# Performance work log

Measured on AMD Instinct MI355X. Metric: run time of the kernel, lower is better.

## Reference

```python
import jax, jax.numpy as jnp
import numpy as np

NPOINT = 1024   # number of sampled centers
NSAMPLE = 32    # neighbors per center
BN_EPS = 1e-5


def setup_inputs() -> dict:
    key = jax.random.key(0)
    ks = jax.random.split(key, 6)
    B, N, C = 8, 4096, 6
    inp = {
        "xyz": jax.random.normal(ks[0], (B, N, 3), jnp.float32),
        "points": jax.random.normal(ks[1], (B, N, C), jnp.float32),
        "W0": jax.random.normal(ks[2], (64, 9), jnp.float32) * 0.1,
        "g0": jnp.ones((64,), jnp.float32),
        "b0": jnp.zeros((64,), jnp.float32),
        "W1": jax.random.normal(ks[3], (64, 64), jnp.float32) * 0.1,
        "g1": jnp.ones((64,), jnp.float32),
        "b1": jnp.zeros((64,), jnp.float32),
        "W2": jax.random.normal(ks[4], (128, 64), jnp.float32) * 0.1,
        "g2": jnp.ones((128,), jnp.float32),
        "b2": jnp.zeros((128,), jnp.float32),
    }
    return inp


def sample_and_group(xyz, points):
    # xyz: [B,N,3], points: [B,N,C]
    B, N, _ = xyz.shape
    stride = N // NPOINT
    new_xyz = xyz[:, ::stride]                      # [B,S,3] deterministic subsample (FPS surrogate)
    # squared pairwise distances via ||a||^2 + ||b||^2 - 2 a.b  -> [B,S,N]
    d = (jnp.sum(new_xyz * new_xyz, -1)[:, :, None]
         + jnp.sum(xyz * xyz, -1)[:, None, :]
         - 2.0 * jnp.einsum('bsd,bnd->bsn', new_xyz, xyz))
    _, idx = jax.lax.top_k(-d, NSAMPLE)             # [B,S,K] KNN indices
    gather = jax.vmap(lambda arr, i: arr[i])        # per-batch gather: [N,C],[S,K] -> [S,K,C]
    g_xyz = gather(xyz, idx) - new_xyz[:, :, None, :]   # relative coords [B,S,K,3]
    g_pts = gather(points, idx)                     # [B,S,K,C]
    new_points = jnp.concatenate([g_xyz, g_pts], -1)    # [B,S,K,3+C]
    return new_xyz, new_points


def mlp_layer(x, W, g, b):
    # Conv2d(1x1, bias=False) == channel contraction; BN2d with batch stats; ReLU
    x = jnp.einsum('bskc,oc->bsko', x, W)
    m = jnp.mean(x, axis=(0, 1, 2))
    v = jnp.var(x, axis=(0, 1, 2))
    x = (x - m) * jax.lax.rsqrt(v + BN_EPS) * g + b
    return jax.nn.relu(x)


def reference(xyz, points, W0, g0, b0, W1, g1, b1, W2, g2, b2):
    new_xyz, x = sample_and_group(xyz, points)      # x: [B,S,K,9]
    x = mlp_layer(x, W0, g0, b0)
    x = mlp_layer(x, W1, g1, b1)
    x = mlp_layer(x, W2, g2, b2)
    new_points = jnp.max(x, axis=2)                 # max-pool over neighbor dim K -> [B,S,128]
    return new_xyz, new_points
```

## Files before the change

### kernel.cpp

```cpp
#include <hip/hip_runtime.h>
#include <float.h>
#include <stdint.h>

#define TOT   262144
#define NPTS  4096
#define KNN   32
#define BN_EPS 1e-5f
#define CAPV  64

typedef _Float16 f16;
typedef _Float16 f16x2 __attribute__((ext_vector_type(2)));
typedef _Float16 f16x4 __attribute__((ext_vector_type(4)));
typedef _Float16 f16x8 __attribute__((ext_vector_type(8)));
typedef float    f32x4 __attribute__((ext_vector_type(4)));

__device__ __forceinline__ int mbcnt64(unsigned long long m){
  return __builtin_amdgcn_mbcnt_hi((unsigned)(m>>32),
         __builtin_amdgcn_mbcnt_lo((unsigned)(m & 0xffffffffull), 0));
}
__device__ __forceinline__ unsigned f2ord(float f){
  unsigned u = __float_as_uint(f);
  return u ^ (((unsigned)((int)u >> 31)) | 0x80000000u);
}
__device__ __forceinline__ f16x2 bnrelu2(f16x2 x, f16x2 a, f16x2 c){
  f16x2 r = x*a + c;
  const f16 z = (f16)0.f;
  r[0] = r[0] > z ? r[0] : z;
  r[1] = r[1] > z ? r[1] : z;
  return r;
}

__global__ __launch_bounds__(256) void prep(const float* __restrict__ xyz,
    float4* __restrict__ xyzp){
  int p = blockIdx.x*256 + threadIdx.x;
  float x = xyz[p*3+0], y = xyz[p*3+1], z = xyz[p*3+2];
  xyzp[p] = make_float4(x, y, z, x*x+y*y+z*z);
}

__global__ __launch_bounds__(256) void knn_gather(
    const float4* __restrict__ xyzp, const float* __restrict__ pts,
    float* __restrict__ grouped, float* __restrict__ out_newxyz){
  __shared__ unsigned skey[4*CAPV];
  __shared__ unsigned short sidx[4*CAPV];
  const int lane = threadIdx.x & 63;
  const int wv   = threadIdx.x >> 6;
  const int q = blockIdx.x*4 + wv;
  const int b = q >> 10, s = q & 1023;
  const float4* xb = xyzp + b*NPTS;
  const float4 Q = xb[s*4];
  const float qx=Q.x, qy=Q.y, qz=Q.z, qq=Q.w;
  if (lane==0){ out_newxyz[q*3]=qx; out_newxyz[q*3+1]=qy; out_newxyz[q*3+2]=qz; }

  unsigned m = 0xFFFFFFFFu;
  #pragma unroll 8
  for (int j=0;j<64;j++){
    float4 P = xb[j*64+lane];
    float d = (qq+P.w) - 2.f*(qx*P.x+qy*P.y+qz*P.z);
    unsigned k = f2ord(d);
    m = k<m ? k : m;
  }
  unsigned sm = m;
  #pragma unroll
  for (int k=2;k<=64;k<<=1){
    #pragma unroll
    for (int j=k>>1;j>0;j>>=1){
      unsigned o = __shfl_xor(sm, j, 64);
      bool keepmin = (((lane&k)==0) == ((lane&j)==0));
      sm = keepmin ? (sm<o?sm:o) : (sm>o?sm:o);
    }
  }
  const unsigned U = __shfl(sm, 31, 64);

  unsigned* wk = skey + wv*CAPV;
  unsigned short* wi = sidx + wv*CAPV;
  int cnt = 0;
  #pragma unroll 4
  for (int j=0;j<64;j++){
    float4 P = xb[j*64+lane];
    float d = (qq+P.w) - 2.f*(qx*P.x+qy*P.y+qz*P.z);
    unsigned k = f2ord(d);
    bool sel = (k <= U);
    unsigned long long msk = __ballot(sel);
    int pos = cnt + mbcnt64(msk);
    if (sel && pos < CAPV){ wk[pos]=k; wi[pos]=(unsigned short)(j*64+lane); }
    cnt += __popcll(msk);
  }

  const float* fb = pts + (size_t)b*NPTS*6;
  const int ebase = q*KNN;
  int n = -1;

  if (cnt <= CAPV){
    unsigned myk = (lane<cnt) ? wk[lane] : 0xFFFFFFFFu;
    unsigned myi = (lane<cnt) ? wi[lane] : 0u;
    unsigned long long v = (((unsigned long long)myk)<<16) | myi;
    #pragma unroll
    for (int k=2;k<=64;k<<=1){
      #pragma unroll
      for (int j=k>>1;j>0;j>>=1){
        unsigned long long o = __shfl_xor(v, j, 64);
        bool keepmin = (((lane&k)==0) == ((lane&j)==0));
        v = keepmin ? (v<o?v:o) : (v>o?v:o);
      }
    }
    if (lane < KNN) n = (int)(v & 0xffffull);
  } else {
    unsigned V=0;
    for (int bit=31; bit>=0; --bit){
      unsigned X = V | (1u<<bit);
      int c=0;
      for (int j=0;j<64;j++){
        float4 P = xb[j*64+lane];
        float d = (qq+P.w) - 2.f*(qx*P.x+qy*P.y+qz*P.z);
        c += __popcll(__ballot(f2ord(d) < X));
      }
      if (c < KNN) V = X;
    }
    int cnt2=0;
    for (int pass=0; pass<2; ++pass){
      for (int j=0;j<64;j++){
        float4 P = xb[j*64+lane];
        float d = (qq+P.w) - 2.f*(qx*P.x+qy*P.y+qz*P.z);
        unsigned kk = f2ord(d);
        bool sel = pass ? (kk==V) : (kk<V);
        unsigned long long msk = __ballot(sel);
        int pos = cnt2 + mbcnt64(msk);
        if (sel && pos < KNN){
          int nn = j*64+lane, e = ebase+pos;
          grouped[0*TOT+e]=P.x-qx; grouped[1*TOT+e]=P.y-qy; grouped[2*TOT+e]=P.z-qz;
          for (int c6=0;c6<6;c6++) grouped[(3+c6)*TOT+e]=fb[nn*6+c6];
        }
        cnt2 += __popcll(msk);
      }
    }
  }
  if (n >= 0){
    float4 P = xb[n];
    int e = ebase + lane;
    grouped[0*TOT+e]=P.x-qx; grouped[1*TOT+e]=P.y-qy; grouped[2*TOT+e]=P.z-qz;
    #pragma unroll
    for (int c6=0;c6<6;c6++) grouped[(3+c6)*TOT+e]=fb[n*6+c6];
  }
}

__global__ __launch_bounds__(256) void stats0(
    const float* __restrict__ grouped, float* __restrict__ s0g){
  const int tid = threadIdx.x, lane = tid&63, wv = tid>>6;
  float v[54];
  #pragma unroll
  for (int i=0;i<54;i++) v[i]=0.f;
  #pragma unroll 1
  for (int it=0; it<2; ++it){
    int n = it*(512*256) + blockIdx.x*256 + tid;
    float g[9];
    #pragma unroll
    for (int c=0;c<9;c++) g[c] = grouped[c*TOT+n];
    #pragma unroll
    for (int c=0;c<9;c++) v[c] += g[c];
    int t=9;
    #pragma unroll
    for (int c=0;c<9;c++)
      #pragma unroll
      for (int c2=0;c2<=c;c2++){ v[t] += g[c]*g[c2]; t++; }
  }
  __shared__ float lds[4][54];
  #pragma unroll
  for (int i=0;i<54;i++){
    float r = v[i];
    #pragma unroll
    for (int off=32; off; off>>=1) r += __shfl_xor(r, off, 64);
    if (lane==0) lds[wv][i]=r;
  }
  __syncthreads();
  if (tid < 54) atomicAdd(&s0g[tid], lds[0][tid]+lds[1][tid]+lds[2][tid]+lds[3][tid]);
}

__global__ void finalize0(const float* __restrict__ s0g,
    const float* __restrict__ W0, const float* __restrict__ g0,
    const float* __restrict__ b0, float* __restrict__ ac0,
    const float* __restrict__ W1, const float* __restrict__ W2,
    f16* __restrict__ W0h, f16* __restrict__ W1h, f16* __restrict__ W2h){
  const int tid = threadIdx.x;
  __shared__ float S[54];
  __shared__ float A0s[64];
  if (tid < 54) S[tid] = s0g[tid];
  __syncthreads();
  if (tid < 64){
    float w[9];
    #pragma unroll
    for (int c=0;c<9;c++) w[c]=W0[tid*9+c];
    float m=0.f;
    #pragma unroll
    for (int c=0;c<9;c++) m += w[c]*S[c];
    float e2=0.f; int t=9;
    #pragma unroll
    for (int c=0;c<9;c++)
      #pragma unroll
      for (int c2=0;c2<=c;c2++){
        float x = w[c]*w[c2]*S[t++];
        e2 += (c2==c) ? x : 2.f*x;
      }
    const float inv = 1.f/(float)TOT;
    m *= inv; e2 *= inv;
    float var = e2 - m*m;
    float a = g0[tid]*rsqrtf(var + BN_EPS);
    ac0[tid]    = a;
    ac0[64+tid] = fmaf(-m, a, b0[tid]);
    A0s[tid]    = a;
  }
  __syncthreads();
  for (int i=tid; i<2048; i+=256){
    int o = i>>5, c = i&31;
    W0h[i] = (f16)(c<9 ? A0s[o]*W0[o*9+c] : 0.f);
  }
  for (int i=tid; i<4096; i+=256) W1h[i] = (f16)W1[i];
  for (int i=tid; i<8192; i+=256) W2h[i] = (f16)W2[i];
}

__global__ __launch_bounds__(256) void layer1(
    const float* __restrict__ grouped, const f16* __restrict__ W0h,
    const f16* __restrict__ W1h, const float* __restrict__ ac0,
    f16* __restrict__ x1h){
  __shared__ f16 hb[4][16][80];
  const int lane = threadIdx.x & 63, wv = threadIdx.x >> 6;
  const int e16 = lane & 15, q = lane >> 4;
  const int base = blockIdx.x*256 + wv*64;

  f16x8 A0[4];
  #pragma unroll
  for (int m=0;m<4;m++) A0[m] = *(const f16x8*)(W0h + (m*16+e16)*32 + q*8);
  f16x8 A1[4][2];
  #pragma unroll
  for (int m=0;m<4;m++)
    #pragma unroll
    for (int s=0;s<2;s++) A1[m][s] = *(const f16x8*)(W1h + (m*16+e16)*64 + s*32 + q*8);
  float c0i[4][4];
  #pragma unroll
  for (int m=0;m<4;m++)
    #pragma unroll
    for (int i=0;i<4;i++) c0i[m][i] = ac0[64 + m*16 + q*4 + i];

  #pragma unroll 1
  for (int sub=0; sub<4; ++sub){
    int elem = base + sub*16 + e16;
    f16x8 bg = {};
    if (q==0){
      #pragma unroll
      for (int j=0;j<8;j++) bg[j] = (f16)grouped[j*TOT + elem];
    } else if (q==1){
      bg[0] = (f16)grouped[8*TOT + elem];
    }
    #pragma unroll
    for (int m=0;m<4;m++){
      f32x4 acc = {c0i[m][0], c0i[m][1], c0i[m][2], c0i[m][3]};
      acc = __builtin_amdgcn_mfma_f32_16x16x32_f16(A0[m], bg, acc, 0,0,0);
      f16x4 w;
      w[0]=(f16)fmaxf(acc[0],0.f); w[1]=(f16)fmaxf(acc[1],0.f);
      w[2]=(f16)fmaxf(acc[2],0.f); w[3]=(f16)fmaxf(acc[3],0.f);
      *(f16x4*)(&hb[wv][e16][m*16 + q*4]) = w;
    }
    f32x4 acc2[4];
    #pragma unroll
    for (int m=0;m<4;m++) acc2[m] = (f32x4){0.f,0.f,0.f,0.f};
    #pragma unroll
    for (int s=0;s<2;s++){
      f16x8 bh = *(const f16x8*)(&hb[wv][e16][s*32 + q*8]);
      #pragma unroll
      for (int m=0;m<4;m++)
        acc2[m] = __builtin_amdgcn_mfma_f32_16x16x32_f16(A1[m][s], bh, acc2[m], 0,0,0);
    }
    #pragma unroll
    for (int m=0;m<4;m++){
      f16x4 w;
      w[0]=(f16)acc2[m][0]; w[1]=(f16)acc2[m][1];
      w[2]=(f16)acc2[m][2]; w[3]=(f16)acc2[m][3];
      *(f16x4*)(x1h + (size_t)elem*64 + m*16 + q*4) = w;
    }
  }
}

__global__ __launch_bounds__(256) void stats1(const f16x8* __restrict__ x1h,
    float* __restrict__ s1g){
  const int tid=threadIdx.x;
  float s[8], qv[8];
  #pragma unroll
  for (int i=0;i<8;i++){ s[i]=0.f; qv[i]=0.f; }
  int base = blockIdx.x*256 + tid;
  #pragma unroll 1
  for (int r=0;r<16;r++){
    f16x8 v = x1h[base + r*131072];
    #pragma unroll
    for (int i=0;i<8;i++){ float f=(float)v[i]; s[i]+=f; qv[i]=fmaf(f,f,qv[i]); }
  }
  __shared__ float lds[256][16];
  #pragma unroll
  for (int i=0;i<8;i++){ lds[tid][i]=s[i]; lds[tid][8+i]=qv[i]; }
  __syncthreads();
  if (tid < 128){
    int c = tid & 63, kind = tid>>6;
    int ph = c>>3, r = (c&7) + (kind?8:0);
    float v=0.f;
    #pragma unroll
    for (int k2=0;k2<32;k2++) v += lds[ph + k2*8][r];
    atomicAdd(&s1g[kind*64+c], v);
  }
}

__global__ void finalizeS(const float* __restrict__ sums, int nch,
    const float* __restrict__ gg, const float* __restrict__ bb,
    float* __restrict__ ac, f16* __restrict__ ach){
  int t=threadIdx.x;
  if (t<nch){
    const float inv=1.f/(float)TOT;
    float m=sums[t]*inv;
    float v=sums[nch+t]*inv - m*m;
    float a=gg[t]*rsqrtf(v+BN_EPS);
    float c=fmaf(-m,a,bb[t]);
    ac[t]=a; ac[nch+t]=c;
    if (ach){ ach[t]=(f16)a; ach[nch+t]=(f16)c; }
  }
}

__global__ __launch_bounds__(256) void layer2max(const f16* __restrict__ x1h,
    const f16* __restrict__ W2h, const f16* __restrict__ ac1h,
    float* __restrict__ maxbuf, float* __restrict__ s2g){
  const int lane = threadIdx.x & 63, wv = threadIdx.x >> 6;
  const int e16 = lane & 15, q = lane >> 4;
  f16x8 Bw[8][2];
  #pragma unroll
  for (int nt=0;nt<8;nt++)
    #pragma unroll
    for (int s=0;s<2;s++) Bw[nt][s] = *(const f16x8*)(W2h + (nt*16+e16)*64 + s*32 + q*8);
  f16x2 a1p[8], c1p[8];
  #pragma unroll
  for (int s=0;s<2;s++)
    #pragma unroll
    for (int j2=0;j2<4;j2++){
      a1p[s*4+j2] = ((const f16x2*)ac1h)[s*16 + q*4 + j2];
      c1p[s*4+j2] = ((const f16x2*)(ac1h+64))[s*16 + q*4 + j2];
    }
  float ssum[8], ssq[8];
  #pragma unroll
  for (int i=0;i<8;i++){ ssum[i]=0.f; ssq[i]=0.f; }

  #pragma unroll 1
  for (int qq=0; qq<4; ++qq){
    const int qid = blockIdx.x*16 + wv*4 + qq;
    f32x4 acc[8][2];
    #pragma unroll
    for (int nt=0;nt<8;nt++){ acc[nt][0]=(f32x4){0,0,0,0}; acc[nt][1]=(f32x4){0,0,0,0}; }
    #pragma unroll
    for (int mt=0; mt<2; ++mt){
      #pragma unroll
      for (int s=0;s<2;s++){
        f16x8 a = *(const f16x8*)(x1h + (size_t)(qid*32 + mt*16 + e16)*64 + s*32 + q*8);
        f16x2* a2 = (f16x2*)&a;
        #pragma unroll
        for (int j2=0;j2<4;j2++) a2[j2] = bnrelu2(a2[j2], a1p[s*4+j2], c1p[s*4+j2]);
        #pragma unroll
        for (int nt=0;nt<8;nt++)
          acc[nt][mt] = __builtin_amdgcn_mfma_f32_16x16x32_f16(a, Bw[nt][s], acc[nt][mt], 0,0,0);
      }
    }
    float mx[8];
    #pragma unroll
    for (int nt=0;nt<8;nt++){
      f32x4 u = acc[nt][0], v = acc[nt][1];
      float m1 = fmaxf(fmaxf(u[0],u[1]), fmaxf(u[2],u[3]));
      float m2 = fmaxf(fmaxf(v[0],v[1]), fmaxf(v[2],v[3]));
      mx[nt] = fmaxf(m1, m2);
      ssum[nt] += (u[0]+u[1])+(u[2]+u[3]) + (v[0]+v[1])+(v[2]+v[3]);
      float sq = 0.f;
      #pragma unroll
      for (int i=0;i<4;i++){ sq = fmaf(u[i],u[i],sq); sq = fmaf(v[i],v[i],sq); }
      ssq[nt] += sq;
      mx[nt] = fmaxf(mx[nt], __shfl_xor(mx[nt], 16, 64));
      mx[nt] = fmaxf(mx[nt], __shfl_xor(mx[nt], 32, 64));
    }
    if (lane < 16){
      #pragma unroll
      for (int nt=0;nt<8;nt++) maxbuf[(size_t)qid*128 + nt*16 + lane] = mx[nt];
    }
  }
  #pragma unroll
  for (int nt=0;nt<8;nt++){
    ssum[nt] += __shfl_xor(ssum[nt], 16, 64);
    ssum[nt] += __shfl_xor(ssum[nt], 32, 64);
    ssq[nt]  += __shfl_xor(ssq[nt], 16, 64);
    ssq[nt]  += __shfl_xor(ssq[nt], 32, 64);
  }
  __shared__ float lds[4][256];
  if (q==0){
    #pragma unroll
    for (int nt=0;nt<8;nt++){
      lds[wv][nt*16+e16]     = ssum[nt];
      lds[wv][128+nt*16+e16] = ssq[nt];
    }
  }
  __syncthreads();
  const int tid = threadIdx.x;
  float v = lds[0][tid]+lds[1][tid]+lds[2][tid]+lds[3][tid];
  atomicAdd(&s2g[tid], v);
}

__global__ __launch_bounds__(256) void apply2(
    const float* __restrict__ maxbuf, const float* __restrict__ ac2,
    float* __restrict__ outp){
  int i = blockIdx.x*256 + threadIdx.x;
  int o = i & 127;
  outp[i] = fmaxf(fmaf(maxbuf[i], ac2[o], ac2[128+o]), 0.f);
}

extern "C" void kernel_launch(void* const* d_in, const int* in_sizes, int n_in,
                              void* d_out, int out_size, void* d_ws, size_t ws_size,
                              hipStream_t stream){
  const float* xyz = (const float*)d_in[0];
  const float* pts = (const float*)d_in[1];
  const float* W0  = (const float*)d_in[2];
  const float* g0  = (const float*)d_in[3];
  const float* b0  = (const float*)d_in[4];
  const float* W1  = (const float*)d_in[5];
  const float* g1  = (const float*)d_in[6];
  const float* b1  = (const float*)d_in[7];
  const float* W2  = (const float*)d_in[8];
  const float* g2  = (const float*)d_in[9];
  const float* b2  = (const float*)d_in[10];
  float* out = (float*)d_out;

  float* ws      = (float*)d_ws;
  float* grouped = ws;
  f16*   x1h     = (f16*)(ws + (size_t)9*TOT);
  float* maxbuf  = ws + (size_t)41*TOT;
  float4* xyzp   = (float4*)(ws + (size_t)45*TOT);
  float* basep   = ws + (size_t)45*TOT + 131072;
  f16*   W0h     = (f16*)basep;
  f16*   W1h     = (f16*)(basep + 1024);
  f16*   W2h     = (f16*)(basep + 3072);
  float* s0g     = basep + 7168;
  float* s1g     = s0g + 64;
  float* s2g     = s1g + 128;
  float* ac0     = s2g + 256;
  float* ac1     = ac0 + 128;
  f16*   ac1h    = (f16*)(ac1 + 128);
  float* ac2     = ac1 + 192;

  (void)hipMemsetAsync(s0g, 0, (64+128+256)*sizeof(float), stream);
  prep      <<< 128, 256, 0, stream>>>(xyz, xyzp);
  knn_gather<<<2048, 256, 0, stream>>>(xyzp, pts, grouped, out);
  stats0    <<< 512, 256, 0, stream>>>(grouped, s0g);
  finalize0 <<<   1, 256, 0, stream>>>(s0g, W0, g0, b0, ac0, W1, W2, W0h, W1h, W2h);
  layer1    <<<1024, 256, 0, stream>>>(grouped, W0h, W1h, ac0, x1h);
  stats1    <<< 512, 256, 0, stream>>>((const f16x8*)x1h, s1g);
  finalizeS <<<   1, 128, 0, stream>>>(s1g,  64, g1, b1, ac1, ac1h);
  layer2max <<< 512, 256, 0, stream>>>(x1h, W2h, ac1h, maxbuf, s2g);
  finalizeS <<<   1, 128, 0, stream>>>(s2g, 128, g2, b2, ac2, (f16*)0);
  apply2    <<<4096, 256, 0, stream>>>(maxbuf, ac2, out + 24576);
}
```

Measured before the change: 231.2 us.

## Fuse layer-1 BN statistics into layer1, store grouped features as fp16

Removes the separate stats1 kernel by accumulating per-channel sum and sum-of-squares of the layer-1 output inside layer1, reduced with shuffles and LDS, then atomically added. layer1 now processes twice as many elements per block. The grouped buffer changes from fp32 to fp16, halving its write and read traffic. The KNN candidate compaction switches from ballot-prefix to LDS atomic counters. Stats are now computed from fp32 accumulators before rounding, and fp16 grouped coordinates lose precision for stats0 and layer0.

```diff
diff --git a/kernel.cpp b/kernel.cpp
--- a/kernel.cpp
+++ b/kernel.cpp
@@ -14,10 +14,6 @@
 typedef _Float16 f16x8 __attribute__((ext_vector_type(8)));
 typedef float    f32x4 __attribute__((ext_vector_type(4)));
 
-__device__ __forceinline__ int mbcnt64(unsigned long long m){
-  return __builtin_amdgcn_mbcnt_hi((unsigned)(m>>32),
-         __builtin_amdgcn_mbcnt_lo((unsigned)(m & 0xffffffffull), 0));
-}
 __device__ __forceinline__ unsigned f2ord(float f){
   unsigned u = __float_as_uint(f);
   return u ^ (((unsigned)((int)u >> 31)) | 0x80000000u);
@@ -39,9 +35,10 @@
 
 __global__ __launch_bounds__(256) void knn_gather(
     const float4* __restrict__ xyzp, const float* __restrict__ pts,
-    float* __restrict__ grouped, float* __restrict__ out_newxyz){
+    f16* __restrict__ grouped, float* __restrict__ out_newxyz){
   __shared__ unsigned skey[4*CAPV];
   __shared__ unsigned short sidx[4*CAPV];
+  __shared__ unsigned lcnt[4];
   const int lane = threadIdx.x & 63;
   const int wv   = threadIdx.x >> 6;
   const int q = blockIdx.x*4 + wv;
@@ -49,7 +46,8 @@
   const float4* xb = xyzp + b*NPTS;
   const float4 Q = xb[s*4];
   const float qx=Q.x, qy=Q.y, qz=Q.z, qq=Q.w;
-  if (lane==0){ out_newxyz[q*3]=qx; out_newxyz[q*3+1]=qy; out_newxyz[q*3+2]=qz; }
+  if (lane==0){ out_newxyz[q*3]=qx; out_newxyz[q*3+1]=qy; out_newxyz[q*3+2]=qz;
+                lcnt[wv]=0; }
 
   unsigned m = 0xFFFFFFFFu;
   #pragma unroll 8
@@ -73,18 +71,17 @@
 
   unsigned* wk = skey + wv*CAPV;
   unsigned short* wi = sidx + wv*CAPV;
-  int cnt = 0;
   #pragma unroll 4
   for (int j=0;j<64;j++){
     float4 P = xb[j*64+lane];
     float d = (qq+P.w) - 2.f*(qx*P.x+qy*P.y+qz*P.z);
     unsigned k = f2ord(d);
-    bool sel = (k <= U);
-    unsigned long long msk = __ballot(sel);
-    int pos = cnt + mbcnt64(msk);
-    if (sel && pos < CAPV){ wk[pos]=k; wi[pos]=(unsigned short)(j*64+lane); }
-    cnt += __popcll(msk);
-  }
+    if (k <= U){
+      unsigned p = atomicAdd(&lcnt[wv], 1u);
+      if (p < CAPV){ wk[p]=k; wi[p]=(unsigned short)(j*64+lane); }
+    }
+  }
+  int cnt = (int)lcnt[wv];
 
   const float* fb = pts + (size_t)b*NPTS*6;
   const int ebase = q*KNN;
@@ -124,11 +121,13 @@
         unsigned kk = f2ord(d);
         bool sel = pass ? (kk==V) : (kk<V);
         unsigned long long msk = __ballot(sel);
-        int pos = cnt2 + mbcnt64(msk);
+        int pos = cnt2 + __builtin_amdgcn_mbcnt_hi((unsigned)(msk>>32),
+                  __builtin_amdgcn_mbcnt_lo((unsigned)(msk & 0xffffffffull), 0));
         if (sel && pos < KNN){
           int nn = j*64+lane, e = ebase+pos;
-          grouped[0*TOT+e]=P.x-qx; grouped[1*TOT+e]=P.y-qy; grouped[2*TOT+e]=P.z-qz;
-          for (int c6=0;c6<6;c6++) grouped[(3+c6)*TOT+e]=fb[nn*6+c6];
+          grouped[0*TOT+e]=(f16)(P.x-qx); grouped[1*TOT+e]=(f16)(P.y-qy);
+          grouped[2*TOT+e]=(f16)(P.z-qz);
+          for (int c6=0;c6<6;c6++) grouped[(3+c6)*TOT+e]=(f16)fb[nn*6+c6];
         }
         cnt2 += __popcll(msk);
       }
@@ -137,14 +136,15 @@
   if (n >= 0){
     float4 P = xb[n];
     int e = ebase + lane;
-    grouped[0*TOT+e]=P.x-qx; grouped[1*TOT+e]=P.y-qy; grouped[2*TOT+e]=P.z-qz;
-    #pragma unroll
-    for (int c6=0;c6<6;c6++) grouped[(3+c6)*TOT+e]=fb[n*6+c6];
+    grouped[0*TOT+e]=(f16)(P.x-qx); grouped[1*TOT+e]=(f16)(P.y-qy);
+    grouped[2*TOT+e]=(f16)(P.z-qz);
+    #pragma unroll
+    for (int c6=0;c6<6;c6++) grouped[(3+c6)*TOT+e]=(f16)fb[n*6+c6];
   }
 }
 
 __global__ __launch_bounds__(256) void stats0(
-    const float* __restrict__ grouped, float* __restrict__ s0g){
+    const f16* __restrict__ grouped, float* __restrict__ s0g){
   const int tid = threadIdx.x, lane = tid&63, wv = tid>>6;
   float v[54];
   #pragma unroll
@@ -154,7 +154,7 @@
     int n = it*(512*256) + blockIdx.x*256 + tid;
     float g[9];
     #pragma unroll
-    for (int c=0;c<9;c++) g[c] = grouped[c*TOT+n];
+    for (int c=0;c<9;c++) g[c] = (float)grouped[c*TOT+n];
     #pragma unroll
     for (int c=0;c<9;c++) v[c] += g[c];
     int t=9;
@@ -218,13 +218,14 @@
 }
 
 __global__ __launch_bounds__(256) void layer1(
-    const float* __restrict__ grouped, const f16* __restrict__ W0h,
+    const f16* __restrict__ grouped, const f16* __restrict__ W0h,
     const f16* __restrict__ W1h, const float* __restrict__ ac0,
-    f16* __restrict__ x1h){
+    f16* __restrict__ x1h, float* __restrict__ s1g){
   __shared__ f16 hb[4][16][80];
+  __shared__ float sred[4][128];
   const int lane = threadIdx.x & 63, wv = threadIdx.x >> 6;
   const int e16 = lane & 15, q = lane >> 4;
-  const int base = blockIdx.x*256 + wv*64;
+  const int base = blockIdx.x*512 + wv*128;
 
   f16x8 A0[4];
   #pragma unroll
@@ -239,16 +240,19 @@
   for (int m=0;m<4;m++)
     #pragma unroll
     for (int i=0;i<4;i++) c0i[m][i] = ac0[64 + m*16 + q*4 + i];
+  float ssum[16], ssq[16];
+  #pragma unroll
+  for (int i=0;i<16;i++){ ssum[i]=0.f; ssq[i]=0.f; }
 
   #pragma unroll 1
-  for (int sub=0; sub<4; ++sub){
+  for (int sub=0; sub<8; ++sub){
     int elem = base + sub*16 + e16;
     f16x8 bg = {};
     if (q==0){
       #pragma unroll
-      for (int j=0;j<8;j++) bg[j] = (f16)grouped[j*TOT + elem];
+      for (int j=0;j<8;j++) bg[j] = grouped[j*TOT + elem];
     } else if (q==1){
-      bg[0] = (f16)grouped[8*TOT + elem];
+      bg[0] = grouped[8*TOT + elem];
     }
     #pragma unroll
     for (int m=0;m<4;m++){
@@ -272,37 +276,41 @@
     #pragma unroll
     for (int m=0;m<4;m++){
       f16x4 w;
-      w[0]=(f16)acc2[m][0]; w[1]=(f16)acc2[m][1];
-      w[2]=(f16)acc2[m][2]; w[3]=(f16)acc2[m][3];
+      #pragma unroll
+      for (int i=0;i<4;i++){
+        float x = acc2[m][i];
+        ssum[m*4+i] += x;
+        ssq[m*4+i]  = fmaf(x, x, ssq[m*4+i]);
+        w[i] = (f16)x;
+      }
       *(f16x4*)(x1h + (size_t)elem*64 + m*16 + q*4) = w;
     }
   }
-}
-
-__global__ __launch_bounds__(256) void stats1(const f16x8* __restrict__ x1h,
-    float* __restrict__ s1g){
-  const int tid=threadIdx.x;
-  float s[8], qv[8];
-  #pragma unroll
-  for (int i=0;i<8;i++){ s[i]=0.f; qv[i]=0.f; }
-  int base = blockIdx.x*256 + tid;
-  #pragma unroll 1
-  for (int r=0;r<16;r++){
-    f16x8 v = x1h[base + r*131072];
-    #pragma unroll
-    for (int i=0;i<8;i++){ float f=(float)v[i]; s[i]+=f; qv[i]=fmaf(f,f,qv[i]); }
-  }
-  __shared__ float lds[256][16];
-  #pragma unroll
-  for (int i=0;i<8;i++){ lds[tid][i]=s[i]; lds[tid][8+i]=qv[i]; }
+  #pragma unroll
+  for (int t=0;t<16;t++){
+    float a = ssum[t], bq = ssq[t];
+    #pragma unroll
+    for (int off=1; off<16; off<<=1){
+      a  += __shfl_xor(a,  off, 64);
+      bq += __shfl_xor(bq, off, 64);
+    }
+    ssum[t]=a; ssq[t]=bq;
+  }
+  if (e16==0){
+    #pragma unroll
+    for (int m=0;m<4;m++)
+      #pragma unroll
+      for (int i=0;i<4;i++){
+        int ch = m*16 + q*4 + i;
+        sred[wv][ch]    = ssum[m*4+i];
+        sred[wv][64+ch] = ssq[m*4+i];
+      }
+  }
   __syncthreads();
+  const int tid = threadIdx.x;
   if (tid < 128){
-    int c = tid & 63, kind = tid>>6;
-    int ph = c>>3, r = (c&7) + (kind?8:0);
-    float v=0.f;
-    #pragma unroll
-    for (int k2=0;k2<32;k2++) v += lds[ph + k2*8][r];
-    atomicAdd(&s1g[kind*64+c], v);
+    float v = sred[0][tid]+sred[1][tid]+sred[2][tid]+sred[3][tid];
+    atomicAdd(&s1g[tid], v);
   }
 }
 
@@ -428,11 +436,11 @@
   float* out = (float*)d_out;
 
   float* ws      = (float*)d_ws;
-  float* grouped = ws;
-  f16*   x1h     = (f16*)(ws + (size_t)9*TOT);
-  float* maxbuf  = ws + (size_t)41*TOT;
-  float4* xyzp   = (float4*)(ws + (size_t)45*TOT);
-  float* basep   = ws + (size_t)45*TOT + 131072;
+  f16*   grouped = (f16*)ws;
+  f16*   x1h     = (f16*)(ws + (size_t)5*TOT);
+  float* maxbuf  = ws + (size_t)37*TOT;
+  float4* xyzp   = (float4*)(ws + (size_t)41*TOT);
+  float* basep   = ws + (size_t)41*TOT + 131072;
   f16*   W0h     = (f16*)basep;
   f16*   W1h     = (f16*)(basep + 1024);
   f16*   W2h     = (f16*)(basep + 3072);
@@ -449,8 +457,7 @@
   knn_gather<<<2048, 256, 0, stream>>>(xyzp, pts, grouped, out);
   stats0    <<< 512, 256, 0, stream>>>(grouped, s0g);
   finalize0 <<<   1, 256, 0, stream>>>(s0g, W0, g0, b0, ac0, W1, W2, W0h, W1h, W2h);
-  layer1    <<<1024, 256, 0, stream>>>(grouped, W0h, W1h, ac0, x1h);
-  stats1    <<< 512, 256, 0, stream>>>((const f16x8*)x1h, s1g);
+  layer1    <<< 512, 256, 0, stream>>>(grouped, W0h, W1h, ac0, x1h, s1g);
   finalizeS <<<   1, 128, 0, stream>>>(s1g,  64, g1, b1, ac1, ac1h);
   layer2max <<< 512, 256, 0, stream>>>(x1h, W2h, ac1h, maxbuf, s2g);
   finalizeS <<<   1, 128, 0, stream>>>(s2g, 128, g2, b2, ac2, (f16*)0);
```

After: 222.3 us. -3.8%, faster.
